# Optimization experiments

Measured on AMD Instinct MI355X. Metric: run time of the kernel, lower is better.

## Reference

```python
import jax, jax.numpy as jnp
import numpy as np

DIM, HEADS = 1024, 16
HD = DIM // HEADS  # head_dim = 64
EPS = 1e-5


def setup_inputs() -> dict:
    key = jax.random.key(0)
    ks = jax.random.split(key, 8)
    B, N = 2, 2048
    x = jax.random.normal(ks[0], (B, N, DIM), dtype=jnp.float32)
    # RoPE table: [N, HD//2, 2] = (cos, sin) per position/freq
    inv_freq = 1.0 / (10000.0 ** (jnp.arange(0, HD, 2, dtype=jnp.float32) / HD))  # [HD//2]
    angles = jnp.arange(N, dtype=jnp.float32)[:, None] * inv_freq[None, :]        # [N, HD//2]
    freq_cis = jnp.stack([jnp.cos(angles), jnp.sin(angles)], axis=-1)             # [N, HD//2, 2]
    s = 0.02
    Wqkv = jax.random.normal(ks[1], (DIM, 3 * DIM), dtype=jnp.float32) * s
    ln_q_g = jnp.ones((HD,), jnp.float32)
    ln_q_b = jnp.zeros((HD,), jnp.float32)
    ln_k_g = jnp.ones((HD,), jnp.float32)
    ln_k_b = jnp.zeros((HD,), jnp.float32)
    Wproj = jax.random.normal(ks[2], (DIM, DIM), dtype=jnp.float32) * s
    bproj = jnp.zeros((DIM,), jnp.float32)
    return {"x": x, "freq_cis": freq_cis, "Wqkv": Wqkv,
            "ln_q_g": ln_q_g, "ln_q_b": ln_q_b, "ln_k_g": ln_k_g, "ln_k_b": ln_k_b,
            "Wproj": Wproj, "bproj": bproj}


def _layernorm(t, g, b):
    mu = jnp.mean(t, axis=-1, keepdims=True)
    var = jnp.mean(jnp.square(t - mu), axis=-1, keepdims=True)
    return (t - mu) * jax.lax.rsqrt(var + EPS) * g + b


def _rope(t, cos, sin):
    # t: [b, n, h, hd]; pairs are interleaved (even=real, odd=imag)
    b, n, h, hd = t.shape
    tr = jnp.transpose(t[..., 0::2], (0, 2, 1, 3))  # [b, h, n, hd//2]
    ti = jnp.transpose(t[..., 1::2], (0, 2, 1, 3))
    out_r = tr * cos - ti * sin
    out_i = tr * sin + ti * cos
    return jnp.stack([out_r, out_i], axis=-1).reshape(b, h, n, hd)  # [b, h, n, hd]


def reference(x, freq_cis, Wqkv, ln_q_g, ln_q_b, ln_k_g, ln_k_b, Wproj, bproj):
    B, N, _ = x.shape
    qkv = (x @ Wqkv).reshape(B, N, 3, HEADS, HD)  # split is outermost in the packed dim
    q, k, v = qkv[:, :, 0], qkv[:, :, 1], qkv[:, :, 2]  # [b, n, h, hd]
    q = _layernorm(q, ln_q_g, ln_q_b)
    k = _layernorm(k, ln_k_g, ln_k_b)
    cos = freq_cis[None, None, :, :, 0]  # [1, 1, n, hd//2]
    sin = freq_cis[None, None, :, :, 1]
    q = _rope(q, cos, sin)  # [b, h, n, hd]
    k = _rope(k, cos, sin)
    v = jnp.transpose(v, (0, 2, 1, 3))  # [b, h, n, hd]
    scores = jnp.einsum('bhqd,bhkd->bhqk', q, k) * (1.0 / np.sqrt(HD))
    attn = jax.nn.softmax(scores, axis=-1)
    out = jnp.einsum('bhqk,bhkd->bhqd', attn, v)
    out = jnp.transpose(out, (0, 2, 1, 3)).reshape(B, N, HEADS * HD)
    return out @ Wproj + bproj
```

## Files before the change

### kernel.cpp

```cpp
#include <hip/hip_runtime.h>

typedef __bf16 bf16_t;
typedef bf16_t bf16x8 __attribute__((ext_vector_type(8)));
typedef bf16_t bf16x4 __attribute__((ext_vector_type(4)));
typedef float f32x4 __attribute__((ext_vector_type(4)));
typedef short s16x4 __attribute__((ext_vector_type(4)));

typedef __attribute__((address_space(1))) void* as1_void;
typedef __attribute__((address_space(3))) void* as3_void;

static constexpr int kDim   = 1024;
static constexpr int kHeads = 16;
static constexpr int kHd    = 64;
static constexpr int kBatch = 2;
static constexpr int kSeq   = 2048;
static constexpr int kM     = kBatch * kSeq;
static constexpr int kNqkv  = 3 * kDim;
static constexpr float kQScale = 0.125f * 1.4426950408889634f;
static constexpr float kFixedMax = 16.0f;

__device__ __forceinline__ void gld_lds16(const bf16_t* g, bf16_t* l) {
  __builtin_amdgcn_global_load_lds((as1_void)(void*)const_cast<bf16_t*>(g),
                                   (as3_void)(void*)l, 16, 0, 0);
}

__device__ __forceinline__ unsigned cvtpk_bf16(float lo, float hi) {
  unsigned r;
  asm("v_cvt_pk_bf16_f32 %0, %1, %2" : "=v"(r) : "v"(lo), "v"(hi));
  return r;
}

__global__ __launch_bounds__(256) void prep(const float* __restrict__ x, bf16_t* __restrict__ xb,
                                            const float* __restrict__ Wqkv, bf16_t* __restrict__ WqkvT,
                                            const float* __restrict__ Wproj, bf16_t* __restrict__ WprojT) {
  __shared__ float tile[32][33];
  const int bid = blockIdx.x, tid = threadIdx.x;
  if (bid < 1024) {
#pragma unroll
    for (int j = 0; j < 4; ++j) {
      const int i = bid * 1024 + j * 256 + tid;
      const float4 f = ((const float4*)x)[i];
      bf16x4 o;
      o[0] = (bf16_t)f.x; o[1] = (bf16_t)f.y; o[2] = (bf16_t)f.z; o[3] = (bf16_t)f.w;
      ((bf16x4*)xb)[i] = o;
    }
    return;
  }
  const float* in; bf16_t* out; int R, C, t;
  if (bid < 4096) { in = Wqkv;  out = WqkvT;  R = kDim; C = kNqkv; t = bid - 1024; }
  else            { in = Wproj; out = WprojT; R = kDim; C = kDim;  t = bid - 4096; }
  const int ntx = C / 32;
  const int c0 = (t % ntx) * 32, r0 = (t / ntx) * 32;
  const int tx = tid & 31, ty = tid >> 5;
#pragma unroll
  for (int j = 0; j < 4; ++j)
    tile[ty + 8 * j][tx] = in[(size_t)(r0 + ty + 8 * j) * C + (c0 + tx)];
  __syncthreads();
#pragma unroll
  for (int j = 0; j < 4; ++j)
    out[(size_t)(c0 + ty + 8 * j) * R + (r0 + tx)] = (bf16_t)tile[tx][ty + 8 * j];
}

__global__ __launch_bounds__(256) void gemm_proj_64(const bf16_t* __restrict__ A,
                                                    const bf16_t* __restrict__ Bt,
                                                    float* __restrict__ Cout,
                                                    const float* __restrict__ bias) {
  const int N = kDim, K = kDim;
  __shared__ __align__(16) bf16_t lA[2][2048];
  __shared__ __align__(16) bf16_t lB[2][4096];
  const int tid  = threadIdx.x;
  const int w    = tid >> 6, lane = tid & 63;
  const int quad = lane >> 4, l16 = lane & 15;
  const int m0 = blockIdx.y * 64, n0 = blockIdx.x * 128;

  const int strow = tid >> 2;
  const int stcol = (tid & 3) * 8;
  const bf16_t* gA = A  + (size_t)(m0 + strow) * K + stcol;
  const bf16_t* gB = Bt + (size_t)(n0 + strow) * K + stcol;

  f32x4 acc[4][2];
#pragma unroll
  for (int i = 0; i < 4; ++i)
#pragma unroll
    for (int j = 0; j < 2; ++j)
#pragma unroll
      for (int r = 0; r < 4; ++r) acc[i][j][r] = 0.f;

  auto stage = [&](int buf, int k0) {
    gld_lds16(gA + k0, &lA[buf][w * 512]);
    gld_lds16(gB + k0, &lB[buf][w * 512]);
    gld_lds16(gB + (size_t)64 * K + k0, &lB[buf][2048 + w * 512]);
  };

  const int nK = K >> 5;
  stage(0, 0);
  __syncthreads();

  for (int kb = 0; kb < nK; ++kb) {
    const int cur = kb & 1;
    if (kb + 1 < nK) stage(cur ^ 1, (kb + 1) * 32);
    bf16x8 af[4], bfr[2];
#pragma unroll
    for (int mt = 0; mt < 4; ++mt)
      af[mt] = *(const bf16x8*)(&lA[cur][(mt * 16 + l16) * 32 + quad * 8]);
#pragma unroll
    for (int nt = 0; nt < 2; ++nt)
      bfr[nt] = *(const bf16x8*)(&lB[cur][(w * 32 + nt * 16 + l16) * 32 + quad * 8]);
#pragma unroll
    for (int mt = 0; mt < 4; ++mt)
#pragma unroll
      for (int nt = 0; nt < 2; ++nt)
        acc[mt][nt] = __builtin_amdgcn_mfma_f32_16x16x32_bf16(af[mt], bfr[nt], acc[mt][nt], 0, 0, 0);
    __syncthreads();
  }

#pragma unroll
  for (int mt = 0; mt < 4; ++mt)
#pragma unroll
    for (int nt = 0; nt < 2; ++nt)
#pragma unroll
      for (int r = 0; r < 4; ++r) {
        const int row = m0 + mt * 16 + quad * 4 + r;
        const int col = n0 + w * 32 + nt * 16 + l16;
        Cout[(size_t)row * N + col] = acc[mt][nt][r] + bias[col];
      }
}

__global__ __launch_bounds__(256, 3) void gemm_qkv_fused(
    const bf16_t* __restrict__ A, const bf16_t* __restrict__ Bt,
    const float* __restrict__ freq,
    const float* __restrict__ gq, const float* __restrict__ bq,
    const float* __restrict__ gk, const float* __restrict__ bk,
    bf16_t* __restrict__ Q, bf16_t* __restrict__ Kout, bf16_t* __restrict__ Vt) {
  __shared__ __align__(16) char smem[34816];
  bf16_t* lA = (bf16_t*)smem;
  bf16_t* lB = lA + 8192;
  const int tid  = threadIdx.x;
  const int w    = tid >> 6, lane = tid & 63;
  const int quad = lane >> 4, l16 = lane & 15;
  const int wm = w >> 1, wn = w & 1;
  const int m0 = blockIdx.y * 128, n0 = blockIdx.x * 128;
  const int K = kDim;

  const int strow = tid >> 2;
  const int stcol = (tid & 3) * 8;
  const bf16_t* gA = A  + (size_t)(m0 + strow) * K + stcol;
  const bf16_t* gB = Bt + (size_t)(n0 + strow) * K + stcol;

  f32x4 acc[4][4];
#pragma unroll
  for (int i = 0; i < 4; ++i)
#pragma unroll
    for (int j = 0; j < 4; ++j)
#pragma unroll
      for (int r = 0; r < 4; ++r) acc[i][j][r] = 0.f;

  auto stage = [&](int buf, int k0) {
    gld_lds16(gA + k0,                  lA + buf * 4096 + w * 512);
    gld_lds16(gA + (size_t)64 * K + k0, lA + buf * 4096 + 2048 + w * 512);
    gld_lds16(gB + k0,                  lB + buf * 4096 + w * 512);
    gld_lds16(gB + (size_t)64 * K + k0, lB + buf * 4096 + 2048 + w * 512);
  };

  const int nK = K >> 5;
  stage(0, 0);
  __syncthreads();

  for (int kb = 0; kb < nK; ++kb) {
    const int cur = kb & 1;
    if (kb + 1 < nK) stage(cur ^ 1, (kb + 1) * 32);
    bf16x8 af[4], bfr[4];
#pragma unroll
    for (int mt = 0; mt < 4; ++mt)
      af[mt] = *(const bf16x8*)(lA + cur * 4096 + (wm * 64 + mt * 16 + l16) * 32 + quad * 8);
#pragma unroll
    for (int nt = 0; nt < 4; ++nt)
      bfr[nt] = *(const bf16x8*)(lB + cur * 4096 + (wn * 64 + nt * 16 + l16) * 32 + quad * 8);
#pragma unroll
    for (int mt = 0; mt < 4; ++mt)
#pragma unroll
      for (int nt = 0; nt < 4; ++nt)
        acc[mt][nt] = __builtin_amdgcn_mfma_f32_16x16x32_bf16(af[mt], bfr[nt], acc[mt][nt], 0, 0, 0);
    __syncthreads();
  }

  const int mat = n0 >> 10;
  const int cin = (n0 & 1023) + wn * 64;
  const int h   = cin >> 6;
  const int bb  = m0 >> 11;
  const int bh  = bb * kHeads + h;
  const int nrow0 = (m0 & 2047) + wm * 64;

  if (mat == 2) {
#pragma unroll
    for (int mt = 0; mt < 4; ++mt)
#pragma unroll
      for (int nt = 0; nt < 4; ++nt) {
        bf16x4 pk;
#pragma unroll
        for (int r = 0; r < 4; ++r) pk[r] = (bf16_t)acc[mt][nt][r];
        const int d = nt * 16 + l16;
        *(bf16x4*)(Vt + ((size_t)bh * kHd + d) * kSeq + nrow0 + mt * 16 + quad * 4) = pk;
      }
    return;
  }

  __syncthreads();
  float* fsm = (float*)smem;
  {
    const int row = tid >> 1, half = tid & 1;
    const float4* src = (const float4*)(freq + ((size_t)(m0 & 2047) + row) * 64 + half * 32);
    float4* dst4 = (float4*)(fsm + row * 68 + half * 32);
#pragma unroll
    for (int j = 0; j < 8; ++j) dst4[j] = src[j];
  }
  __syncthreads();

  const float* gv_ = (mat == 0) ? gq : gk;
  const float* bv_ = (mat == 0) ? bq : bk;
  float gv[4], bv[4];
#pragma unroll
  for (int nt = 0; nt < 4; ++nt) { gv[nt] = gv_[nt * 16 + l16]; bv[nt] = bv_[nt * 16 + l16]; }
  bf16_t* dst = (mat == 0) ? Q : Kout;
  const float sgn = (l16 & 1) ? 1.f : -1.f;
  const float scl = (mat == 0) ? kQScale : 1.f;

#pragma unroll
  for (int mt = 0; mt < 4; ++mt) {
    float mu[4], inv[4];
#pragma unroll
    for (int r = 0; r < 4; ++r) {
      float s = acc[mt][0][r] + acc[mt][1][r] + acc[mt][2][r] + acc[mt][3][r];
      s += __shfl_xor(s, 1); s += __shfl_xor(s, 2);
      s += __shfl_xor(s, 4); s += __shfl_xor(s, 8);
      mu[r] = s * (1.f / 64.f);
    }
#pragma unroll
    for (int r = 0; r < 4; ++r) {
      float vs = 0.f;
#pragma unroll
      for (int nt = 0; nt < 4; ++nt) {
        const float dd = acc[mt][nt][r] - mu[r];
        vs += dd * dd;
      }
      vs += __shfl_xor(vs, 1); vs += __shfl_xor(vs, 2);
      vs += __shfl_xor(vs, 4); vs += __shfl_xor(vs, 8);
      inv[r] = rsqrtf(vs * (1.f / 64.f) + 1e-5f);
    }
#pragma unroll
    for (int nt = 0; nt < 4; ++nt) {
#pragma unroll
      for (int r = 0; r < 4; ++r) {
        const float y = (acc[mt][nt][r] - mu[r]) * inv[r] * gv[nt] + bv[nt];
        const float part = __shfl_xor(y, 1);
        const int mloc = wm * 64 + mt * 16 + quad * 4 + r;
        const float2 cs = *(const float2*)(fsm + mloc * 68 + ((nt * 16 + l16) & ~1));
        const float outv = (y * cs.x + sgn * part * cs.y) * scl;
        dst[((size_t)bh * kSeq + nrow0 + mt * 16 + quad * 4 + r) * kHd + nt * 16 + l16] =
            (bf16_t)outv;
      }
    }
  }
}

__global__ __launch_bounds__(256, 4) void flash_attn13(const bf16_t* __restrict__ Q,
                                                       const bf16_t* __restrict__ K,
                                                       const bf16_t* __restrict__ Vt,
                                                       bf16_t* __restrict__ Op0,
                                                       bf16_t* __restrict__ Op1,
                                                       float* __restrict__ rsum) {
  __shared__ __align__(16) bf16_t lK[2][4096];
  __shared__ __align__(16) bf16_t lV[2][4096];
  const int tid  = threadIdx.x;
  const int w    = tid >> 6, lane = tid & 63;
  const int quad = lane >> 4, l16 = lane & 15;
  const int bh = blockIdx.x & 31;
  const int t2 = blockIdx.x >> 5;
  const int qb = t2 & 15;
  const int sp = t2 >> 4;
  const int b = bh >> 4, h = bh & 15;
  const int q0 = qb * 128 + w * 32;
  const int kv0 = sp * (kSeq / 2);
  const bf16_t* Qb = Q  + (size_t)bh * kSeq * kHd;
  const bf16_t* Kb = K  + (size_t)bh * kSeq * kHd + (size_t)kv0 * kHd;
  const bf16_t* Vb = Vt + (size_t)bh * kHd * kSeq + kv0;

  bf16x8 qf[2][2];
#pragma unroll
  for (int nt = 0; nt < 2; ++nt)
#pragma unroll
    for (int ks = 0; ks < 2; ++ks)
      qf[nt][ks] = *(const bf16x8*)(Qb + (size_t)(q0 + nt * 16 + l16) * kHd + ks * 32 + quad * 8);

  bf16x8 ones8;
#pragma unroll
  for (int j = 0; j < 8; ++j) ones8[j] = (bf16_t)((l16 == 0) ? 1.0f : 0.0f);

  const int r0s = (w * 2 + 0) * 8 + (lane >> 3);
  const int r1s = (w * 2 + 1) * 8 + (lane >> 3);
  const int ch  = lane & 7;
  const bf16_t* kS0 = Kb + (size_t)r0s * kHd + (ch ^ (r0s & 7)) * 8;
  const bf16_t* kS1 = Kb + (size_t)r1s * kHd + (ch ^ (r1s & 7)) * 8;
  const bf16_t* vS0 = Vb + (size_t)r0s * kSeq + (ch ^ (r0s & 7)) * 8;
  const bf16_t* vS1 = Vb + (size_t)r1s * kSeq + (ch ^ (r1s & 7)) * 8;
  bf16_t* dK0 = &lK[0][(w * 2 + 0) * 512];
  bf16_t* dK1 = &lK[0][(w * 2 + 1) * 512];
  bf16_t* dV0 = &lV[0][(w * 2 + 0) * 512];
  bf16_t* dV1 = &lV[0][(w * 2 + 1) * 512];

  auto stage = [&](int buf, int tile) {
    gld_lds16(kS0 + (size_t)tile * 4096, dK0 + buf * 4096);
    gld_lds16(kS1 + (size_t)tile * 4096, dK1 + buf * 4096);
    gld_lds16(vS0 + (size_t)tile * 64,   dV0 + buf * 4096);
    gld_lds16(vS1 + (size_t)tile * 64,   dV1 + buf * 4096);
  };

  f32x4 o[4][2];
  f32x4 osum[2];
#pragma unroll
  for (int nt = 0; nt < 2; ++nt) {
#pragma unroll
    for (int r = 0; r < 4; ++r) osum[nt][r] = 0.f;
#pragma unroll
    for (int ntd = 0; ntd < 4; ++ntd)
#pragma unroll
      for (int r = 0; r < 4; ++r) o[ntd][nt][r] = 0.f;
  }

  const int nIter = kSeq / 128;

  stage(0, 0);
  __syncthreads();

  for (int it = 0; it < nIter; ++it) {
    const int cur = it & 1;
    if (it + 1 < nIter) stage(cur ^ 1, it + 1);

#pragma unroll
    for (int pr = 0; pr < 2; ++pr) {
      unsigned pbu[2][2][2];
#pragma unroll
      for (int sub = 0; sub < 2; ++sub) {
        const int krow = pr * 32 + (l16 >> 2) * 8 + sub * 4 + (l16 & 3);
        const int swl  = sub * 4 + (l16 & 3);
        const bf16x8 kf0 = *(const bf16x8*)(&lK[cur][krow * 64 + (quad ^ swl) * 8]);
        const bf16x8 kf1 = *(const bf16x8*)(&lK[cur][krow * 64 + ((4 + quad) ^ swl) * 8]);
#pragma unroll
        for (int nt = 0; nt < 2; ++nt) {
          f32x4 st;
#pragma unroll
          for (int r = 0; r < 4; ++r) st[r] = -kFixedMax;
          st = __builtin_amdgcn_mfma_f32_16x16x32_bf16(kf0, qf[nt][0], st, 0, 0, 0);
          st = __builtin_amdgcn_mfma_f32_16x16x32_bf16(kf1, qf[nt][1], st, 0, 0, 0);
          pbu[sub][nt][0] = cvtpk_bf16(exp2f(st[0]), exp2f(st[1]));
          pbu[sub][nt][1] = cvtpk_bf16(exp2f(st[2]), exp2f(st[3]));
        }
      }
#pragma unroll
      for (int nt = 0; nt < 2; ++nt) {
        uint4 u = {pbu[0][nt][0], pbu[0][nt][1], pbu[1][nt][0], pbu[1][nt][1]};
        const bf16x8 pfr = __builtin_bit_cast(bf16x8, u);
#pragma unroll
        for (int ntd = 0; ntd < 4; ++ntd) {
          const int vrow = ntd * 16 + l16;
          const bf16x8 va = *(const bf16x8*)(&lV[cur][vrow * 64 +
                                                      ((pr * 4 + quad) ^ (vrow & 7)) * 8]);
          o[ntd][nt] = __builtin_amdgcn_mfma_f32_16x16x32_bf16(va, pfr, o[ntd][nt], 0, 0, 0);
        }
        osum[nt] = __builtin_amdgcn_mfma_f32_16x16x32_bf16(ones8, pfr, osum[nt], 0, 0, 0);
      }
    }
    __syncthreads();
  }

  if (quad == 0) {
#pragma unroll
    for (int nt = 0; nt < 2; ++nt)
      rsum[((size_t)sp * 32 + bh) * kSeq + q0 + nt * 16 + l16] = osum[nt][0];
  }

  bf16_t* op = sp ? Op1 : Op0;
#pragma unroll
  for (int nt = 0; nt < 2; ++nt) {
    const int row = q0 + nt * 16 + l16;
#pragma unroll
    for (int ntd = 0; ntd < 4; ++ntd) {
      bf16x4 ov;
#pragma unroll
      for (int r = 0; r < 4; ++r) ov[r] = (bf16_t)o[ntd][nt][r];
      *(bf16x4*)(op + ((size_t)(b * kSeq + row)) * kDim + h * kHd + ntd * 16 + quad * 4) = ov;
    }
  }
}

__global__ __launch_bounds__(256) void combine(bf16_t* __restrict__ p0,
                                               const bf16_t* __restrict__ p1,
                                               const float* __restrict__ rs) {
  const int tid = threadIdx.x;
  const int row = blockIdx.x * 2 + (tid >> 7);
  const int col = (tid & 127) * 8;
  const int h = col >> 6;
  const int b = row >> 11;
  const int r = row & 2047;
  const int bh = b * kHeads + h;
  const float inv = 1.f / (rs[(size_t)bh * kSeq + r] + rs[(size_t)(32 + bh) * kSeq + r]);
  const size_t idx = (size_t)row * kDim + col;
  const bf16x8 a = *(const bf16x8*)(p0 + idx);
  const bf16x8 c = *(const bf16x8*)(p1 + idx);
  bf16x8 o;
#pragma unroll
  for (int j = 0; j < 8; ++j) o[j] = (bf16_t)(((float)a[j] + (float)c[j]) * inv);
  *(bf16x8*)(p0 + idx) = o;
}

extern "C" void kernel_launch(void* const* d_in, const int* in_sizes, int n_in,
                              void* d_out, int out_size, void* d_ws, size_t ws_size,
                              hipStream_t stream) {
  const float* x     = (const float*)d_in[0];
  const float* freq  = (const float*)d_in[1];
  const float* Wqkv  = (const float*)d_in[2];
  const float* gq    = (const float*)d_in[3];
  const float* bq    = (const float*)d_in[4];
  const float* gk    = (const float*)d_in[5];
  const float* bk    = (const float*)d_in[6];
  const float* Wproj = (const float*)d_in[7];
  const float* bproj = (const float*)d_in[8];
  float* out = (float*)d_out;

  char* ws = (char*)d_ws;
  bf16_t* xb     = (bf16_t*)(ws + 0);
  bf16_t* WqkvT  = (bf16_t*)(ws + 8388608);
  bf16_t* WprojT = (bf16_t*)(ws + 14680064);
  bf16_t* Qb     = (bf16_t*)(ws + 16777216);
  bf16_t* Kb     = (bf16_t*)(ws + 25165824);
  bf16_t* Vtb    = (bf16_t*)(ws + 33554432);
  bf16_t* part0  = (bf16_t*)(ws + 41943040);
  bf16_t* part1  = (bf16_t*)(ws + 0);
  float*  rsum   = (float*)(ws + 8388608);

  prep<<<dim3(5120), dim3(256), 0, stream>>>(x, xb, Wqkv, WqkvT, Wproj, WprojT);
  gemm_qkv_fused<<<dim3(kNqkv / 128, kM / 128), dim3(256), 0, stream>>>(
      xb, WqkvT, freq, gq, bq, gk, bk, Qb, Kb, Vtb);
  flash_attn13<<<dim3((kSeq / 128) * 2 * kBatch * kHeads), dim3(256), 0, stream>>>(
      Qb, Kb, Vtb, part0, part1, rsum);
  combine<<<dim3(kM / 2), dim3(256), 0, stream>>>(part0, part1, rsum);
  gemm_proj_64<<<dim3(kDim / 128, kM / 64), dim3(256), 0, stream>>>(part0, WprojT, out, bproj);
}
```

Baseline: 206.6 us.

## Fuse split-KV combine into projection GEMM A-load and prioritize attention MFMA phases

Removes the separate combine kernel. The projection GEMM now loads both attention partials through registers, sums them, scales each row by the reciprocal softmax denominator precomputed into shared memory, and writes the result to LDS as the A tile. This drops one launch and one full read-write pass over the attention output. The cost is that the A operand no longer uses direct global-to-LDS loads, and the 8 projection blocks sharing a row tile each redo the combine arithmetic. In the attention kernel, V fragments are hoisted ahead of the PV MFMAs and s_setprio brackets the MFMA sections to favor matrix issue across waves.

After: 207.7 us. Within noise of the previous version (+0.5%).

```diff
diff --git a/kernel.cpp b/kernel.cpp
--- a/kernel.cpp
+++ b/kernel.cpp
@@ -61,21 +61,34 @@
     out[(size_t)(c0 + ty + 8 * j) * R + (r0 + tx)] = (bf16_t)tile[tx][ty + 8 * j];
 }
 
-__global__ __launch_bounds__(256) void gemm_proj_64(const bf16_t* __restrict__ A,
-                                                    const bf16_t* __restrict__ Bt,
-                                                    float* __restrict__ Cout,
-                                                    const float* __restrict__ bias) {
+__global__ __launch_bounds__(256) void gemm_proj_fused(const bf16_t* __restrict__ p0,
+                                                       const bf16_t* __restrict__ p1,
+                                                       const float* __restrict__ rs,
+                                                       const bf16_t* __restrict__ Bt,
+                                                       float* __restrict__ Cout,
+                                                       const float* __restrict__ bias) {
   const int N = kDim, K = kDim;
   __shared__ __align__(16) bf16_t lA[2][2048];
   __shared__ __align__(16) bf16_t lB[2][4096];
+  __shared__ float invt[1024];
   const int tid  = threadIdx.x;
   const int w    = tid >> 6, lane = tid & 63;
   const int quad = lane >> 4, l16 = lane & 15;
   const int m0 = blockIdx.y * 64, n0 = blockIdx.x * 128;
 
+#pragma unroll
+  for (int j = 0; j < 4; ++j) {
+    const int e = tid * 4 + j;
+    const int i = e >> 4, h = e & 15;
+    const int row = m0 + i;
+    const int b = row >> 11, r = row & 2047;
+    const int bh = b * kHeads + h;
+    invt[e] = 1.f / (rs[(size_t)bh * kSeq + r] + rs[(size_t)(32 + bh) * kSeq + r]);
+  }
+
   const int strow = tid >> 2;
   const int stcol = (tid & 3) * 8;
-  const bf16_t* gA = A  + (size_t)(m0 + strow) * K + stcol;
+  const size_t aoff = (size_t)(m0 + strow) * K + stcol;
   const bf16_t* gB = Bt + (size_t)(n0 + strow) * K + stcol;
 
   f32x4 acc[4][2];
@@ -86,19 +99,36 @@
 #pragma unroll
       for (int r = 0; r < 4; ++r) acc[i][j][r] = 0.f;
 
-  auto stage = [&](int buf, int k0) {
-    gld_lds16(gA + k0, &lA[buf][w * 512]);
+  auto stageB = [&](int buf, int k0) {
     gld_lds16(gB + k0, &lB[buf][w * 512]);
     gld_lds16(gB + (size_t)64 * K + k0, &lB[buf][2048 + w * 512]);
   };
+  auto writeA = [&](int buf, int kb, bf16x8 a0, bf16x8 a1) {
+    const float inv = invt[strow * 16 + (kb >> 1)];
+    unsigned u[4];
+#pragma unroll
+    for (int p = 0; p < 4; ++p)
+      u[p] = cvtpk_bf16(((float)a0[2 * p] + (float)a1[2 * p]) * inv,
+                        ((float)a0[2 * p + 1] + (float)a1[2 * p + 1]) * inv);
+    uint4 uu = {u[0], u[1], u[2], u[3]};
+    *(uint4*)(&lA[buf][strow * 32 + stcol]) = uu;
+  };
 
   const int nK = K >> 5;
-  stage(0, 0);
+  bf16x8 a0 = *(const bf16x8*)(p0 + aoff);
+  bf16x8 a1 = *(const bf16x8*)(p1 + aoff);
+  stageB(0, 0);
+  __syncthreads();
+  writeA(0, 0, a0, a1);
   __syncthreads();
 
   for (int kb = 0; kb < nK; ++kb) {
     const int cur = kb & 1;
-    if (kb + 1 < nK) stage(cur ^ 1, (kb + 1) * 32);
+    if (kb + 1 < nK) {
+      a0 = *(const bf16x8*)(p0 + aoff + (kb + 1) * 32);
+      a1 = *(const bf16x8*)(p1 + aoff + (kb + 1) * 32);
+      stageB(cur ^ 1, (kb + 1) * 32);
+    }
     bf16x8 af[4], bfr[2];
 #pragma unroll
     for (int mt = 0; mt < 4; ++mt)
@@ -111,6 +141,7 @@
 #pragma unroll
       for (int nt = 0; nt < 2; ++nt)
         acc[mt][nt] = __builtin_amdgcn_mfma_f32_16x16x32_bf16(af[mt], bfr[nt], acc[mt][nt], 0, 0, 0);
+    if (kb + 1 < nK) writeA(cur ^ 1, kb + 1, a0, a1);
     __syncthreads();
   }
 
@@ -263,7 +294,7 @@
   }
 }
 
-__global__ __launch_bounds__(256, 4) void flash_attn13(const bf16_t* __restrict__ Q,
+__global__ __launch_bounds__(256, 4) void flash_attn15(const bf16_t* __restrict__ Q,
                                                        const bf16_t* __restrict__ K,
                                                        const bf16_t* __restrict__ Vt,
                                                        bf16_t* __restrict__ Op0,
@@ -345,6 +376,7 @@
         const int swl  = sub * 4 + (l16 & 3);
         const bf16x8 kf0 = *(const bf16x8*)(&lK[cur][krow * 64 + (quad ^ swl) * 8]);
         const bf16x8 kf1 = *(const bf16x8*)(&lK[cur][krow * 64 + ((4 + quad) ^ swl) * 8]);
+        __builtin_amdgcn_s_setprio(1);
 #pragma unroll
         for (int nt = 0; nt < 2; ++nt) {
           f32x4 st;
@@ -355,20 +387,25 @@
           pbu[sub][nt][0] = cvtpk_bf16(exp2f(st[0]), exp2f(st[1]));
           pbu[sub][nt][1] = cvtpk_bf16(exp2f(st[2]), exp2f(st[3]));
         }
-      }
+        __builtin_amdgcn_s_setprio(0);
+      }
+      bf16x8 va[4];
+#pragma unroll
+      for (int ntd = 0; ntd < 4; ++ntd) {
+        const int vrow = ntd * 16 + l16;
+        va[ntd] = *(const bf16x8*)(&lV[cur][vrow * 64 + ((pr * 4 + quad) ^ (vrow & 7)) * 8]);
+      }
+      __builtin_amdgcn_s_setprio(1);
 #pragma unroll
       for (int nt = 0; nt < 2; ++nt) {
         uint4 u = {pbu[0][nt][0], pbu[0][nt][1], pbu[1][nt][0], pbu[1][nt][1]};
         const bf16x8 pfr = __builtin_bit_cast(bf16x8, u);
 #pragma unroll
-        for (int ntd = 0; ntd < 4; ++ntd) {
-          const int vrow = ntd * 16 + l16;
-          const bf16x8 va = *(const bf16x8*)(&lV[cur][vrow * 64 +
-                                                      ((pr * 4 + quad) ^ (vrow & 7)) * 8]);
-          o[ntd][nt] = __builtin_amdgcn_mfma_f32_16x16x32_bf16(va, pfr, o[ntd][nt], 0, 0, 0);
-        }
+        for (int ntd = 0; ntd < 4; ++ntd)
+          o[ntd][nt] = __builtin_amdgcn_mfma_f32_16x16x32_bf16(va[ntd], pfr, o[ntd][nt], 0, 0, 0);
         osum[nt] = __builtin_amdgcn_mfma_f32_16x16x32_bf16(ones8, pfr, osum[nt], 0, 0, 0);
       }
+      __builtin_amdgcn_s_setprio(0);
     }
     __syncthreads();
   }
@@ -391,26 +428,6 @@
       *(bf16x4*)(op + ((size_t)(b * kSeq + row)) * kDim + h * kHd + ntd * 16 + quad * 4) = ov;
     }
   }
-}
-
-__global__ __launch_bounds__(256) void combine(bf16_t* __restrict__ p0,
-                                               const bf16_t* __restrict__ p1,
-                                               const float* __restrict__ rs) {
-  const int tid = threadIdx.x;
-  const int row = blockIdx.x * 2 + (tid >> 7);
-  const int col = (tid & 127) * 8;
-  const int h = col >> 6;
-  const int b = row >> 11;
-  const int r = row & 2047;
-  const int bh = b * kHeads + h;
-  const float inv = 1.f / (rs[(size_t)bh * kSeq + r] + rs[(size_t)(32 + bh) * kSeq + r]);
-  const size_t idx = (size_t)row * kDim + col;
-  const bf16x8 a = *(const bf16x8*)(p0 + idx);
-  const bf16x8 c = *(const bf16x8*)(p1 + idx);
-  bf16x8 o;
-#pragma unroll
-  for (int j = 0; j < 8; ++j) o[j] = (bf16_t)(((float)a[j] + (float)c[j]) * inv);
-  *(bf16x8*)(p0 + idx) = o;
 }
 
 extern "C" void kernel_launch(void* const* d_in, const int* in_sizes, int n_in,
@@ -441,8 +458,8 @@
   prep<<<dim3(5120), dim3(256), 0, stream>>>(x, xb, Wqkv, WqkvT, Wproj, WprojT);
   gemm_qkv_fused<<<dim3(kNqkv / 128, kM / 128), dim3(256), 0, stream>>>(
       xb, WqkvT, freq, gq, bq, gk, bk, Qb, Kb, Vtb);
-  flash_attn13<<<dim3((kSeq / 128) * 2 * kBatch * kHeads), dim3(256), 0, stream>>>(
+  flash_attn15<<<dim3((kSeq / 128) * 2 * kBatch * kHeads), dim3(256), 0, stream>>>(
       Qb, Kb, Vtb, part0, part1, rsum);
-  combine<<<dim3(kM / 2), dim3(256), 0, stream>>>(part0, part1, rsum);
-  gemm_proj_64<<<dim3(kDim / 128, kM / 64), dim3(256), 0, stream>>>(part0, WprojT, out, bproj);
-}
+  gemm_proj_fused<<<dim3(kDim / 128, kM / 64), dim3(256), 0, stream>>>(
+      part0, part1, rsum, WprojT, out, bproj);
+}
```
